# Kernel tuning notes

Measured on AMD Instinct MI355X. Metric: run time of the kernel, lower is better.

The kernel has to match this reference:

```python
import jax, jax.numpy as jnp
import numpy as np

ALPHA = 0.7
NUM_HEADS = 12
NUM_KV_HEADS = 6
HEAD_DIM = 64
ROPE_BASE = 10000.0


def ternary_quantize(w):
    thr = ALPHA * jnp.mean(jnp.abs(w))
    return jnp.sign(w) * (jnp.abs(w) >= thr).astype(w.dtype)


def bitlinear(x, w):
    # forward: F.linear(x, ternary(w)) * mean(|w|)
    scale = jnp.mean(jnp.abs(w))
    qw = ternary_quantize(w)
    return (x @ qw.T) * scale


def rope_tables(seq_len, dim, dtype):
    inv_freq = 1.0 / (ROPE_BASE ** (jnp.arange(0, dim, 2, dtype=jnp.float32) / dim))
    t = jnp.arange(seq_len, dtype=jnp.float32)
    freqs = jnp.outer(t, inv_freq)            # [S, dim/2]
    emb = jnp.concatenate([freqs, freqs], -1)  # [S, dim]
    return jnp.cos(emb).astype(dtype), jnp.sin(emb).astype(dtype)


def rotate_half(x):
    x1, x2 = jnp.split(x, 2, axis=-1)
    return jnp.concatenate([-x2, x1], axis=-1)


def setup_inputs() -> dict:
    key = jax.random.key(0)
    ks = jax.random.split(key, 5)
    B, S, H = 2, 2048, 768
    return {
        "hidden_states": jax.random.normal(ks[0], (B, S, H), jnp.float32),
        "Wq": jax.random.normal(ks[1], (768, 768), jnp.float32) * 0.02,
        "Wk": jax.random.normal(ks[2], (384, 768), jnp.float32) * 0.02,
        "Wv": jax.random.normal(ks[3], (384, 768), jnp.float32) * 0.02,
        "Wo": jax.random.normal(ks[4], (768, 768), jnp.float32) * 0.02,
    }


def reference(hidden_states, Wq, Wk, Wv, Wo):
    B, S, H = hidden_states.shape
    nh, nkv, hd = NUM_HEADS, NUM_KV_HEADS, HEAD_DIM
    groups = nh // nkv

    q = bitlinear(hidden_states, Wq).reshape(B, S, nh, hd).transpose(0, 2, 1, 3)
    k = bitlinear(hidden_states, Wk).reshape(B, S, nkv, hd).transpose(0, 2, 1, 3)
    v = bitlinear(hidden_states, Wv).reshape(B, S, nkv, hd).transpose(0, 2, 1, 3)

    cos, sin = rope_tables(S, hd, hidden_states.dtype)  # [S, hd]
    cos = cos[None, None]  # [1,1,S,hd]
    sin = sin[None, None]
    q = q * cos + rotate_half(q) * sin
    k = k * cos + rotate_half(k) * sin

    # GQA: expand kv heads to full head count
    k = jnp.repeat(k, groups, axis=1)  # [B, nh, S, hd]
    v = jnp.repeat(v, groups, axis=1)

    scale = 1.0 / jnp.sqrt(jnp.asarray(hd, hidden_states.dtype))
    scores = jnp.einsum("bhsd,bhtd->bhst", q, k) * scale
    attn = jax.nn.softmax(scores, axis=-1)
    out = jnp.einsum("bhst,bhtd->bhsd", attn, v)
    out = out.transpose(0, 2, 1, 3).reshape(B, S, H)
    return bitlinear(out, Wo)
```

## Files before the change

### kernel.cpp

```cpp
#include <hip/hip_runtime.h>
#include <cmath>

typedef unsigned short u16;
typedef unsigned int u32;
typedef __bf16 bf16x2 __attribute__((ext_vector_type(2)));
typedef __bf16 bf16x8 __attribute__((ext_vector_type(8)));
typedef float f32x2 __attribute__((ext_vector_type(2)));
typedef float f32x16 __attribute__((ext_vector_type(16)));

#define NQ (768*768)
#define NK (384*768)

__device__ __forceinline__ u16 f2bf(float f) {
  u32 u = __float_as_uint(f);
  u32 r = (u + 0x7FFFu + ((u >> 16) & 1u)) >> 16;
  return (u16)r;
}
__device__ __forceinline__ u32 packbf(float a, float b) {
#if __has_builtin(__builtin_amdgcn_cvt_pk_bf16_f32)
  bf16x2 v = __builtin_amdgcn_cvt_pk_bf16_f32(a, b);
  u32 r; __builtin_memcpy(&r, &v, 4); return r;
#else
  return (u32)f2bf(a) | ((u32)f2bf(b) << 16);
#endif
}
__device__ __forceinline__ float fexp2(float x) {
#if __has_builtin(__builtin_amdgcn_exp2f)
  return __builtin_amdgcn_exp2f(x);
#else
  return exp2f(x);
#endif
}
__device__ __forceinline__ bf16x8 ldfrag(const u16* p) { bf16x8 v; __builtin_memcpy(&v, p, 16); return v; }
__device__ __forceinline__ f32x16 mfma32_(bf16x8 a, bf16x8 b, f32x16 c) {
  return __builtin_amdgcn_mfma_f32_32x32x16_bf16(a, b, c, 0, 0, 0);
}
__device__ __forceinline__ void gload_lds16(const u16* g, u16* l) {
  __builtin_amdgcn_global_load_lds((const __attribute__((address_space(1))) void*)g,
                                   (__attribute__((address_space(3))) void*)l, 16, 0, 0);
}

__device__ __forceinline__ int fidx(int r, int k) {
  return (r >> 5) * 24576 + (k >> 4) * 512 + ((r & 31) + 32 * ((k >> 3) & 1)) * 8 + (k & 7);
}
__device__ __forceinline__ int kidx(int b6kvh, int s, int d) {
  return b6kvh * 131072 + (s >> 5) * 2048 + (d >> 4) * 512 +
         ((s & 31) + 32 * ((d >> 3) & 1)) * 8 + (d & 7);
}
__device__ __forceinline__ int qidx(int b, int s, int h, int d) {
  return ((b * 64 + (s >> 5)) * 12 + h) * 2048 + (d >> 4) * 512 +
         ((s & 31) + 32 * ((d >> 3) & 1)) * 8 + (d & 7);
}
__device__ __forceinline__ int vidx(int b6kvh, int d, int p) {
  return b6kvh * 131072 + (p >> 6) * 4096 + (d >> 5) * 2048 + ((p >> 4) & 3) * 512 +
         ((d & 31) + 32 * ((p >> 3) & 1)) * 8 + (p & 7);
}

__global__ __launch_bounds__(256) void abssum_kernel(const float* __restrict__ wq, const float* __restrict__ wk,
                                                     const float* __restrict__ wv, const float* __restrict__ wo,
                                                     float* __restrict__ sums) {
  int which = blockIdx.y;
  const float* w = (which == 0) ? wq : (which == 1) ? wk : (which == 2) ? wv : wo;
  int n4 = ((which == 0 || which == 3) ? NQ : NK) >> 2;
  const float4* w4 = (const float4*)w;
  float s = 0.f;
  for (int i = blockIdx.x * blockDim.x + threadIdx.x; i < n4; i += gridDim.x * blockDim.x) {
    float4 v = w4[i];
    s += fabsf(v.x) + fabsf(v.y) + fabsf(v.z) + fabsf(v.w);
  }
  for (int off = 32; off; off >>= 1) s += __shfl_down(s, off);
  __shared__ float ls[4];
  if ((threadIdx.x & 63) == 0) ls[threadIdx.x >> 6] = s;
  __syncthreads();
  if (threadIdx.x == 0) atomicAdd(&sums[which], ls[0] + ls[1] + ls[2] + ls[3]);
}

__global__ __launch_bounds__(256) void prep_kernel(const float* __restrict__ wq, const float* __restrict__ wk,
                                                   const float* __restrict__ wv, const float* __restrict__ wo,
                                                   const float* __restrict__ sums, const float* __restrict__ x,
                                                   u16* __restrict__ qw, u16* __restrict__ woq,
                                                   u16* __restrict__ xb, float2* __restrict__ rt) {
  int i = blockIdx.x * blockDim.x + threadIdx.x;
  if (i < 221184) {
    int n = i / 96, k8 = i - n * 96;
    const float* src; float th; u16* dst; int nd;
    if (n < 768)       { src = wq + n * 768;          th = 0.7f * sums[0] * (1.f / NQ); dst = qw;  nd = n; }
    else if (n < 1152) { src = wk + (n - 768) * 768;  th = 0.7f * sums[1] * (1.f / NK); dst = qw;  nd = n; }
    else if (n < 1536) { src = wv + (n - 1152) * 768; th = 0.7f * sums[2] * (1.f / NK); dst = qw;  nd = n; }
    else               { src = wo + (n - 1536) * 768; th = 0.7f * sums[3] * (1.f / NQ); dst = woq; nd = n - 1536; }
    const float4* sp = (const float4*)(src + k8 * 8);
    float4 v0 = sp[0], v1 = sp[1];
    float e[8] = {v0.x, v0.y, v0.z, v0.w, v1.x, v1.y, v1.z, v1.w};
    u16 o[8];
#pragma unroll
    for (int j = 0; j < 8; j++)
      o[j] = f2bf((fabsf(e[j]) >= th) ? ((e[j] > 0.f) ? 1.f : -1.f) : 0.f);
    __builtin_memcpy(dst + fidx(nd, k8 * 8), o, 16);
  } else if (i < 614400) {
    int j = i - 221184;
    int m = j / 96, k8 = j - m * 96;
    const float4* xp = (const float4*)(x + m * 768 + k8 * 8);
    float4 v0 = xp[0], v1 = xp[1];
    u16 o[8] = { f2bf(v0.x), f2bf(v0.y), f2bf(v0.z), f2bf(v0.w),
                 f2bf(v1.x), f2bf(v1.y), f2bf(v1.z), f2bf(v1.w) };
    __builtin_memcpy(xb + fidx(m, k8 * 8), o, 16);
  } else {
    int j = i - 614400;
    int s = j >> 5, c = j & 31;
    float f = exp2f((float)c * -0.41524101186092029f);
    float sn, cs; sincosf((float)s * f, &sn, &cs);
    rt[j] = make_float2(cs, sn);
  }
}

__global__ __launch_bounds__(256, 2) void gemm_qkv_kernel(const u16* __restrict__ xb, const u16* __restrict__ qw,
                                                          const float* __restrict__ sums,
                                                          const float2* __restrict__ rt,
                                                          u16* __restrict__ qb, u16* __restrict__ kb,
                                                          u16* __restrict__ vT) {
  __shared__ u16 sA[2][4][4][512];
  __shared__ u16 sB[2][4][4][512];
  int tn = blockIdx.x, tm = blockIdx.y;
  int t = threadIdx.x, lane = t & 63, w = t >> 6, c = lane & 31, g2 = lane >> 5;
  int wm = w & 1, wn = w >> 1;

  const u16* asrc = xb + (tm * 4 + w) * 24576 + lane * 8;
  const u16* bsrc = qw + (tn * 4 + w) * 24576 + lane * 8;

  auto stage = [&](int s, int bufi) {
    u16* adst = &sA[bufi][w][0][0];
    u16* bdst = &sB[bufi][w][0][0];
    const u16* ap = asrc + s * 2048;
    const u16* bp = bsrc + s * 2048;
#pragma unroll
    for (int kc = 0; kc < 4; kc++) {
      gload_lds16(ap + kc * 512, adst + kc * 512);
      gload_lds16(bp + kc * 512, bdst + kc * 512);
    }
  };

  f32x16 acc[2][2];
  acc[0][0] = (f32x16)0.f; acc[0][1] = (f32x16)0.f;
  acc[1][0] = (f32x16)0.f; acc[1][1] = (f32x16)0.f;

  stage(0, 0);
  __syncthreads();
  for (int s = 0; s < 12; ++s) {
    int b = s & 1;
    if (s < 11) stage(s + 1, b ^ 1);
#pragma unroll
    for (int kc = 0; kc < 4; kc++) {
      bf16x8 a0 = ldfrag(&sA[b][2 * wm][kc][lane * 8]);
      bf16x8 a1 = ldfrag(&sA[b][2 * wm + 1][kc][lane * 8]);
      bf16x8 b0 = ldfrag(&sB[b][2 * wn][kc][lane * 8]);
      bf16x8 b1 = ldfrag(&sB[b][2 * wn + 1][kc][lane * 8]);
      acc[0][0] = mfma32_(a0, b0, acc[0][0]);
      acc[0][1] = mfma32_(a0, b1, acc[0][1]);
      acc[1][0] = mfma32_(a1, b0, acc[1][0]);
      acc[1][1] = mfma32_(a1, b1, acc[1][1]);
    }
    __syncthreads();
  }

  float sq = sums[0] * (1.f / NQ) * 0.180336880111120f;
  float sk = sums[1] * (1.f / NK);
  float sv = sums[2] * (1.f / NK);
  if (tn < 9) {
    float sc = (tn < 6) ? sq : sk;
    int head = (tn < 6) ? (tn * 2 + wn) : ((tn - 6) * 2 + wn);
    const float2* rp = rt + c;
#pragma unroll
    for (int mi = 0; mi < 2; mi++) {
      int mb = tm * 128 + wm * 64 + mi * 32 + 4 * g2;
#pragma unroll
      for (int r = 0; r < 16; r++) {
        int m = mb + (r & 3) + 8 * (r >> 2);
        int bb = m >> 11, s = m & 2047;
        float2 cs2 = rp[s << 5];
        float x1 = acc[mi][0][r] * sc, x2 = acc[mi][1][r] * sc;
        u16 y1 = f2bf(x1 * cs2.x - x2 * cs2.y);
        u16 y2 = f2bf(x2 * cs2.x + x1 * cs2.y);
        if (tn < 6) {
          qb[qidx(bb, s, head, c)]      = y1;
          qb[qidx(bb, s, head, c + 32)] = y2;
        } else {
          kb[kidx(bb * 6 + head, s, c)]      = y1;
          kb[kidx(bb * 6 + head, s, c + 32)] = y2;
        }
      }
    }
  } else {
    int kvh = (tn - 9) * 2 + wn;
#pragma unroll
    for (int mi = 0; mi < 2; mi++) {
      int mb = tm * 128 + wm * 64 + mi * 32 + 4 * g2;
#pragma unroll
      for (int nb = 0; nb < 2; nb++)
#pragma unroll
        for (int r = 0; r < 16; r++) {
          int m = mb + (r & 3) + 8 * (r >> 2);
          int bb = m >> 11, s = m & 2047;
          int sp = (s & ~12) | ((s & 4) << 1) | ((s & 8) >> 1);
          vT[vidx(bb * 6 + kvh, nb * 32 + c, sp)] = f2bf(acc[mi][nb][r] * sv);
        }
    }
  }
}

__device__ __forceinline__ void attn_step(const bf16x8 (&kf)[4], const bf16x8 (&vf)[2][2],
                                          const bf16x8 (&qf)[4], f32x16 (&O)[2], float& lsum) {
  f32x16 S = (f32x16)0.f;
  __builtin_amdgcn_s_setprio(1);
#pragma unroll
  for (int ks = 0; ks < 4; ks++) S = mfma32_(kf[ks], qf[ks], S);
  __builtin_amdgcn_s_setprio(0);
#pragma unroll
  for (int r = 0; r < 16; r++) S[r] = fexp2(S[r]);
  f32x2 a0 = {S[0], S[1]},  a1 = {S[2], S[3]},  a2 = {S[4], S[5]},  a3 = {S[6], S[7]};
  f32x2 a4 = {S[8], S[9]},  a5 = {S[10], S[11]}, a6 = {S[12], S[13]}, a7 = {S[14], S[15]};
  f32x2 b0 = a0 + a1, b1 = a2 + a3, b2 = a4 + a5, b3 = a6 + a7;
  f32x2 c0 = b0 + b1, c1 = b2 + b3;
  f32x2 d = c0 + c1;
  lsum += d.x + d.y;
  u32 P[8];
#pragma unroll
  for (int j = 0; j < 8; j++) P[j] = packbf(S[2 * j], S[2 * j + 1]);
  bf16x8 PA0, PA1;
  __builtin_memcpy(&PA0, &P[0], 16);
  __builtin_memcpy(&PA1, &P[4], 16);
  __builtin_amdgcn_s_setprio(1);
  O[0] = mfma32_(PA0, vf[0][0], O[0]);
  O[1] = mfma32_(PA0, vf[1][0], O[1]);
  O[0] = mfma32_(PA1, vf[0][1], O[0]);
  O[1] = mfma32_(PA1, vf[1][1], O[1]);
  __builtin_amdgcn_s_setprio(0);
}

__global__ __launch_bounds__(256, 4) void attn_kernel(const u16* __restrict__ qb, const u16* __restrict__ kb,
                                                      const u16* __restrict__ vT, u16* __restrict__ ab) {
  __shared__ float Obuf[4][32][66];
  __shared__ float Lbuf[4][32];
  int bk = blockIdx.x;
  int b = bk / 6, kvh = bk % 6;
  int qp = blockIdx.y & 31, h2 = blockIdx.y >> 5;
  int h = kvh * 2 + h2;
  int t = threadIdx.x, lane = t & 63, w = t >> 6, c = lane & 31, g2 = lane >> 5;
  int qi = w & 1, kh = w >> 1;
  int qt = qp * 2 + qi;

  const u16* qbase = qb + ((b * 64 + qt) * 12 + h) * 2048 + lane * 8;
  bf16x8 qf[4];
#pragma unroll
  for (int ks = 0; ks < 4; ks++) qf[ks] = ldfrag(qbase + ks * 512);

  f32x16 fz = (f32x16)0.f;
  f32x16 O[2] = {fz, fz};
  float lsum = 0.f;

  const u16* Kb = kb + bk * 131072;
  const u16* Vb = vT + bk * 131072;

  for (int it = 0; it < 32; ++it) {
    int g = kh * 32 + it;
    const u16* kt = Kb + g * 2048 + lane * 8;
    const u16* vt = Vb + (g >> 1) * 4096 + (g & 1) * 1024 + lane * 8;
    bf16x8 kf[4], vf[2][2];
#pragma unroll
    for (int ks = 0; ks < 4; ks++) kf[ks] = ldfrag(kt + ks * 512);
#pragma unroll
    for (int dn = 0; dn < 2; dn++)
#pragma unroll
      for (int ksv = 0; ksv < 2; ksv++)
        vf[dn][ksv] = ldfrag(vt + dn * 2048 + ksv * 512);
    attn_step(kf, vf, qf, O, lsum);
  }

  float ltot = lsum + __shfl_xor(lsum, 32);
  if (g2 == 0) Lbuf[w][c] = ltot;
#pragma unroll
  for (int dn = 0; dn < 2; dn++)
#pragma unroll
    for (int r = 0; r < 16; r++)
      Obuf[w][(r & 3) + 8 * (r >> 2) + 4 * g2][dn * 32 + c] = O[dn][r];
  __syncthreads();
  {
    int hn = t >> 7, qq = (t >> 2) & 31, dc = (t & 3) * 16;
    float l = Lbuf[hn][qq] + Lbuf[hn + 2][qq];
    float inv = 1.f / l;
    u16 o[16];
#pragma unroll
    for (int j = 0; j < 16; j++)
      o[j] = f2bf((Obuf[hn][qq][dc + j] + Obuf[hn + 2][qq][dc + j]) * inv);
    int mg = b * 64 + qp * 2 + hn;
    u16* dst = ab + mg * 24576 + ((h * 64 + dc) >> 4) * 512 + qq * 8;
    __builtin_memcpy(dst, o, 16);
    __builtin_memcpy(dst + 256, o + 8, 16);
  }
}

__global__ __launch_bounds__(256, 3) void gemm_out_kernel(const u16* __restrict__ ab, const u16* __restrict__ woq,
                                                          const float* __restrict__ sums, float* __restrict__ out) {
  __shared__ u16 sA[2][4][4][512];
  __shared__ u16 sB[2][2][4][512];
  int tn = blockIdx.x, tm = blockIdx.y;
  int t = threadIdx.x, lane = t & 63, w = t >> 6, c = lane & 31, g2 = lane >> 5;
  int wm = w & 1, wn = w >> 1;

  const u16* asrc = ab + (tm * 4 + w) * 24576 + lane * 8;
  const u16* bsrc = woq + (tn * 2 + (w >> 1)) * 24576 + lane * 8;
  int kc0 = (w & 1) * 2;

  auto stage = [&](int s, int bufi) {
    const u16* ap = asrc + s * 2048;
    u16* adst = &sA[bufi][w][0][0];
#pragma unroll
    for (int kc = 0; kc < 4; kc++) gload_lds16(ap + kc * 512, adst + kc * 512);
    const u16* bp = bsrc + s * 2048;
    u16* bdst = &sB[bufi][w >> 1][0][0];
#pragma unroll
    for (int j = 0; j < 2; j++) gload_lds16(bp + (kc0 + j) * 512, bdst + (kc0 + j) * 512);
  };

  f32x16 acc[2]; acc[0] = (f32x16)0.f; acc[1] = (f32x16)0.f;

  stage(0, 0);
  __syncthreads();
  for (int s = 0; s < 12; ++s) {
    int b = s & 1;
    if (s < 11) stage(s + 1, b ^ 1);
#pragma unroll
    for (int kc = 0; kc < 4; kc++) {
      bf16x8 a0 = ldfrag(&sA[b][2 * wm][kc][lane * 8]);
      bf16x8 a1 = ldfrag(&sA[b][2 * wm + 1][kc][lane * 8]);
      bf16x8 bf = ldfrag(&sB[b][wn][kc][lane * 8]);
      acc[0] = mfma32_(a0, bf, acc[0]);
      acc[1] = mfma32_(a1, bf, acc[1]);
    }
    __syncthreads();
  }

  float so = sums[3] * (1.f / NQ);
#pragma unroll
  for (int mi = 0; mi < 2; mi++) {
    int mb = tm * 128 + wm * 64 + mi * 32 + 4 * g2;
#pragma unroll
    for (int r = 0; r < 16; r++) {
      int m = mb + (r & 3) + 8 * (r >> 2);
      out[m * 768 + tn * 64 + wn * 32 + c] = acc[mi][r] * so;
    }
  }
}

extern "C" void kernel_launch(void* const* d_in, const int* in_sizes, int n_in,
                              void* d_out, int out_size, void* d_ws, size_t ws_size,
                              hipStream_t stream) {
  const float* x  = (const float*)d_in[0];
  const float* wq = (const float*)d_in[1];
  const float* wk = (const float*)d_in[2];
  const float* wv = (const float*)d_in[3];
  const float* wo = (const float*)d_in[4];
  float* out = (float*)d_out;
  char* ws = (char*)d_ws;

  float* sums = (float*)ws;
  u16* qw  = (u16*)(ws + 256);
  u16* woq = (u16*)(ws + 2359552);
  u16* xb  = (u16*)(ws + 3539200);
  u16* qb  = (u16*)(ws + 9830656);
  u16* kb  = (u16*)(ws + 16122112);
  u16* vT  = (u16*)(ws + 19267840);
  u16* ab  = (u16*)(ws + 22413568);
  float2* rt = (float2*)(ws + 28705024);

  hipMemsetAsync(sums, 0, 16, stream);
  dim3 blk(256);
  abssum_kernel<<<dim3(64, 4), blk, 0, stream>>>(wq, wk, wv, wo, sums);
  prep_kernel<<<dim3(2656), blk, 0, stream>>>(wq, wk, wv, wo, sums, x, qw, woq, xb, rt);
  gemm_qkv_kernel<<<dim3(12, 32), blk, 0, stream>>>(xb, qw, sums, rt, qb, kb, vT);
  attn_kernel<<<dim3(12, 64), blk, 0, stream>>>(qb, kb, vT, ab);
  gemm_out_kernel<<<dim3(12, 32), blk, 0, stream>>>(ab, woq, sums, out);
}
```

Baseline: 157.9 us.

## Process two query tiles per wave to reuse K/V fragments across both

Each wave now holds both query tiles of the block and splits the key range four ways instead of two. Every loaded K/V fragment feeds two attention steps, which halves K/V global loads per unit of compute. The cost is higher register pressure (two sets of Q fragments and accumulators), so occupancy drops from 4 to 3 blocks per SM. The epilogue now does a four-way reduction through shared memory, run twice with an extra barrier.

```diff
diff --git a/kernel.cpp b/kernel.cpp
--- a/kernel.cpp
+++ b/kernel.cpp
@@ -236,7 +236,7 @@
   __builtin_amdgcn_s_setprio(0);
 }
 
-__global__ __launch_bounds__(256, 4) void attn_kernel(const u16* __restrict__ qb, const u16* __restrict__ kb,
+__global__ __launch_bounds__(256, 3) void attn_kernel(const u16* __restrict__ qb, const u16* __restrict__ kb,
                                                       const u16* __restrict__ vT, u16* __restrict__ ab) {
   __shared__ float Obuf[4][32][66];
   __shared__ float Lbuf[4][32];
@@ -245,23 +245,22 @@
   int qp = blockIdx.y & 31, h2 = blockIdx.y >> 5;
   int h = kvh * 2 + h2;
   int t = threadIdx.x, lane = t & 63, w = t >> 6, c = lane & 31, g2 = lane >> 5;
-  int qi = w & 1, kh = w >> 1;
-  int qt = qp * 2 + qi;
-
-  const u16* qbase = qb + ((b * 64 + qt) * 12 + h) * 2048 + lane * 8;
-  bf16x8 qf[4];
-#pragma unroll
-  for (int ks = 0; ks < 4; ks++) qf[ks] = ldfrag(qbase + ks * 512);
+
+  const u16* q0 = qb + ((b * 64 + qp * 2) * 12 + h) * 2048 + lane * 8;
+  const u16* q1 = q0 + 12 * 2048;
+  bf16x8 qf0[4], qf1[4];
+#pragma unroll
+  for (int ks = 0; ks < 4; ks++) { qf0[ks] = ldfrag(q0 + ks * 512); qf1[ks] = ldfrag(q1 + ks * 512); }
 
   f32x16 fz = (f32x16)0.f;
-  f32x16 O[2] = {fz, fz};
-  float lsum = 0.f;
+  f32x16 O0[2] = {fz, fz}, O1[2] = {fz, fz};
+  float lsum0 = 0.f, lsum1 = 0.f;
 
   const u16* Kb = kb + bk * 131072;
   const u16* Vb = vT + bk * 131072;
 
-  for (int it = 0; it < 32; ++it) {
-    int g = kh * 32 + it;
+  for (int it = 0; it < 16; ++it) {
+    int g = w * 16 + it;
     const u16* kt = Kb + g * 2048 + lane * 8;
     const u16* vt = Vb + (g >> 1) * 4096 + (g & 1) * 1024 + lane * 8;
     bf16x8 kf[4], vf[2][2];
@@ -272,29 +271,35 @@
 #pragma unroll
       for (int ksv = 0; ksv < 2; ksv++)
         vf[dn][ksv] = ldfrag(vt + dn * 2048 + ksv * 512);
-    attn_step(kf, vf, qf, O, lsum);
-  }
-
-  float ltot = lsum + __shfl_xor(lsum, 32);
-  if (g2 == 0) Lbuf[w][c] = ltot;
-#pragma unroll
-  for (int dn = 0; dn < 2; dn++)
-#pragma unroll
-    for (int r = 0; r < 16; r++)
-      Obuf[w][(r & 3) + 8 * (r >> 2) + 4 * g2][dn * 32 + c] = O[dn][r];
-  __syncthreads();
-  {
-    int hn = t >> 7, qq = (t >> 2) & 31, dc = (t & 3) * 16;
-    float l = Lbuf[hn][qq] + Lbuf[hn + 2][qq];
+    attn_step(kf, vf, qf0, O0, lsum0);
+    attn_step(kf, vf, qf1, O1, lsum1);
+  }
+
+  float lt0 = lsum0 + __shfl_xor(lsum0, 32);
+  float lt1 = lsum1 + __shfl_xor(lsum1, 32);
+
+#pragma unroll
+  for (int qi = 0; qi < 2; qi++) {
+    if (qi) __syncthreads();
+    if (g2 == 0) Lbuf[w][c] = qi ? lt1 : lt0;
+    const f32x16* Ow = qi ? O1 : O0;
+#pragma unroll
+    for (int dn = 0; dn < 2; dn++)
+#pragma unroll
+      for (int r = 0; r < 16; r++)
+        Obuf[w][(r & 3) + 8 * (r >> 2) + 4 * g2][dn * 32 + c] = Ow[dn][r];
+    __syncthreads();
+    int qq = t >> 3, col8 = (t & 7) * 8;
+    float l = Lbuf[0][qq] + Lbuf[1][qq] + Lbuf[2][qq] + Lbuf[3][qq];
     float inv = 1.f / l;
-    u16 o[16];
-#pragma unroll
-    for (int j = 0; j < 16; j++)
-      o[j] = f2bf((Obuf[hn][qq][dc + j] + Obuf[hn + 2][qq][dc + j]) * inv);
-    int mg = b * 64 + qp * 2 + hn;
-    u16* dst = ab + mg * 24576 + ((h * 64 + dc) >> 4) * 512 + qq * 8;
+    u16 o[8];
+#pragma unroll
+    for (int j = 0; j < 8; j++)
+      o[j] = f2bf((Obuf[0][qq][col8 + j] + Obuf[1][qq][col8 + j] +
+                   Obuf[2][qq][col8 + j] + Obuf[3][qq][col8 + j]) * inv);
+    int mg = b * 64 + qp * 2 + qi;
+    u16* dst = ab + mg * 24576 + ((h * 64 + col8) >> 4) * 512 + ((col8 >> 3) & 1) * 256 + qq * 8;
     __builtin_memcpy(dst, o, 16);
-    __builtin_memcpy(dst + 256, o + 8, 16);
   }
 }
 
```

Result: no change. 157.0 us (-0.6%).
